# Optimization experiments

Measured on AMD Instinct MI355X. Metric: run time of the kernel, lower is better.

The kernel has to match this reference:

```python
import jax, jax.numpy as jnp
import numpy as np

B, S, D = 8, 2048, 512
KD = 64          # key_dim == value_dim
WIDTH = 128      # attention_width
NEG = 1.0e9


def setup_inputs() -> dict:
    key = jax.random.key(0)
    ks = jax.random.split(key, 16)
    glorot_dd = float(np.sqrt(6.0 / (D + KD)))
    glorot_sd = float(np.sqrt(6.0 / (S + KD)))
    u = lambda k, shape, lim: jax.random.uniform(k, shape, jnp.float32, -lim, lim)
    return {
        "x": jax.random.normal(ks[0], (B, S, D), jnp.float32),
        "Wqr": u(ks[1], (D, KD), glorot_dd), "bqr": jnp.zeros((KD,), jnp.float32),
        "Wqi": u(ks[2], (D, KD), glorot_dd), "bqi": jnp.zeros((KD,), jnp.float32),
        "Wkr": u(ks[3], (D, KD), glorot_dd), "bkr": jnp.zeros((KD,), jnp.float32),
        "Wki": u(ks[4], (D, KD), glorot_dd), "bki": jnp.zeros((KD,), jnp.float32),
        "Wv": u(ks[5], (D, KD), glorot_dd),  "bv": jnp.zeros((KD,), jnp.float32),
        "pos_qr": u(ks[6], (S, KD), glorot_sd), "pos_qi": u(ks[7], (S, KD), glorot_sd),
        "pos_kr": u(ks[8], (S, KD), glorot_sd), "pos_ki": u(ks[9], (S, KD), glorot_sd),
        "temperature": jnp.ones((1,), jnp.float32),
    }


def _masks():
    ind = jnp.arange(S)
    band = (jnp.abs(ind[:, None] - ind[None, :]) <= WIDTH).astype(jnp.float32)  # [S,S]
    causal = jnp.tril(jnp.ones((S, S), jnp.float32))                            # [S,S]
    return band, causal


def reference(x, Wqr, bqr, Wqi, bqi, Wkr, bkr, Wki, bki, Wv, bv,
              pos_qr, pos_qi, pos_kr, pos_ki, temperature):
    scale = 1.0 / jnp.sqrt(jnp.float32(KD))
    # complex Q/K via two real Dense layers; Q scaled BEFORE adding interference
    qr = (x @ Wqr + bqr) * scale + pos_qr[None]   # [B,S,KD]
    qi = (x @ Wqi + bqi) * scale + pos_qi[None]
    kr = (x @ Wkr + bkr) + pos_kr[None]
    ki = (x @ Wki + bki) + pos_ki[None]
    v = x @ Wv + bv                                # [B,S,KD]
    # real part of complex Q @ K^T (transpose, not conjugate-transpose)
    scores = (jnp.einsum('bsd,btd->bst', qr, kr)
              - jnp.einsum('bsd,btd->bst', qi, ki)) * scale  # [B,S,S]
    band, causal = _masks()
    scores = scores * band - NEG * (1.0 - band)
    scores = scores * causal - NEG * (1.0 - causal)
    probs = jax.nn.softmax(scores * temperature[0], axis=-1)
    return jnp.einsum('bst,btd->bsd', probs, v)
```

## Files before the change

kernel.cpp:

```cpp
#include <hip/hip_runtime.h>

#define NB 8
#define NS 2048
#define ND 512
#define NKD 64
#define NM (NB*NS)

typedef _Float16 f16x8 __attribute__((ext_vector_type(8)));
typedef float f32x4 __attribute__((ext_vector_type(4)));


__global__ __launch_bounds__(256) void wprep_kernel(
    const float* __restrict__ w0, const float* __restrict__ w1,
    const float* __restrict__ w2, const float* __restrict__ w3,
    const float* __restrict__ w4,
    f16x8* __restrict__ wfrag)
{
    const int t = blockIdx.x * 256 + threadIdx.x;
    const int p    = t >> 12;
    const int nf   = (t >> 10) & 3;
    const int kt   = (t >> 6) & 15;
    const int lane = t & 63;
    const float* __restrict__ W = (p==0)?w0:(p==1)?w1:(p==2)?w2:(p==3)?w3:w4;
    const int n  = nf*16 + (lane & 15);
    const int k0 = kt*32 + (lane >> 4)*8;
    f16x8 v;
    #pragma unroll
    for (int j = 0; j < 8; ++j)
        v[j] = (_Float16)W[(size_t)(k0 + j)*NKD + n];
    wfrag[t] = v;
}

__global__ __launch_bounds__(256) void proj_mfma(
    const float* __restrict__ x,
    const f16x8* __restrict__ wfrag,
    const float* __restrict__ b0, const float* __restrict__ b1,
    const float* __restrict__ b2, const float* __restrict__ b3,
    const float* __restrict__ b4,
    const float* __restrict__ p0, const float* __restrict__ p1,
    const float* __restrict__ p2, const float* __restrict__ p3,
    _Float16* __restrict__ qkri,
    _Float16* __restrict__ vT)
{
    __shared__ __align__(16) _Float16 vtile[64][40];

    const int w    = threadIdx.x >> 6;
    const int lane = threadIdx.x & 63;
    const int half = w & 1;
    const int mt   = blockIdx.x*2 + (w >> 1);
    const int m0   = mt * 16;

    const int col   = lane & 15;
    const int rbase = (lane >> 4) << 2;

    const float* __restrict__ xrow = x + (size_t)(m0 + col) * ND + (lane >> 4)*8;
    const f16x8* __restrict__ wf   = wfrag + lane;
    const int pa = half * 2;

    f32x4 acc[2][4], accv[2];
    #pragma unroll
    for (int pp = 0; pp < 2; ++pp)
        #pragma unroll
        for (int nf = 0; nf < 4; ++nf) acc[pp][nf] = (f32x4){0.f,0.f,0.f,0.f};
    accv[0] = (f32x4){0.f,0.f,0.f,0.f};
    accv[1] = (f32x4){0.f,0.f,0.f,0.f};

    for (int kt = 0; kt < 16; ++kt) {
        float4 xa = *(const float4*)(xrow + kt*32);
        float4 xb = *(const float4*)(xrow + kt*32 + 4);
        f16x8 a;
        a[0]=(_Float16)xa.x; a[1]=(_Float16)xa.y;
        a[2]=(_Float16)xa.z; a[3]=(_Float16)xa.w;
        a[4]=(_Float16)xb.x; a[5]=(_Float16)xb.y;
        a[6]=(_Float16)xb.z; a[7]=(_Float16)xb.w;
        #pragma unroll
        for (int pp = 0; pp < 2; ++pp)
            #pragma unroll
            for (int nf = 0; nf < 4; ++nf) {
                f16x8 b = wf[((pa + pp)*4 + nf)*1024 + kt*64];
                acc[pp][nf] = __builtin_amdgcn_mfma_f32_16x16x32_f16(a, b, acc[pp][nf], 0, 0, 0);
            }
        #pragma unroll
        for (int j = 0; j < 2; ++j) {
            const int nfv = half*2 + j;
            f16x8 b = wf[(16 + nfv)*1024 + kt*64];
            accv[j] = __builtin_amdgcn_mfma_f32_16x16x32_f16(a, b, accv[j], 0, 0, 0);
        }
    }

    const float* biases[5] = {b0, b1, b2, b3, b4};
    const float* poss[4]   = {p0, p1, p2, p3};

    #pragma unroll
    for (int pp = 0; pp < 2; ++pp) {
        const int p = pa + pp;
        _Float16* ob = qkri + ((size_t)p*NM + m0) * NKD;
        #pragma unroll
        for (int nf = 0; nf < 4; ++nf) {
            const int c = nf*16 + col;
            const float bb = biases[p][c];
            #pragma unroll
            for (int r = 0; r < 4; ++r) {
                const int mm = rbase + r;
                const int s  = (m0 + mm) & (NS - 1);
                float t = acc[pp][nf][r] + bb;
                if (p < 2) t = t * 0.125f + poss[p][s*NKD + c];
                else       t = t + poss[p][s*NKD + c];
                ob[(size_t)mm*NKD + c] = (_Float16)t;
            }
        }
    }

    #pragma unroll
    for (int j = 0; j < 2; ++j) {
        const int c = (half*2 + j)*16 + col;
        const float bb = b4[c];
        #pragma unroll
        for (int r = 0; r < 4; ++r) {
            const int sl = (w >> 1)*16 + rbase + r;
            vtile[c][sl] = (_Float16)(accv[j][r] + bb);
        }
    }
    __syncthreads();
    {
        const int t   = threadIdx.x;
        const int d   = t >> 2;
        const int sc  = (t & 3) * 8;
        const int mblk = blockIdx.x * 32;
        const int bidx = mblk >> 11;
        const int sb   = mblk & (NS - 1);
        f16x8 vv = *(const f16x8*)&vtile[d][sc];
        *(f16x8*)&vT[((size_t)bidx*NKD + d)*NS + sb + sc] = vv;
    }
}

#define SST 164
#define OST 68

__global__ __launch_bounds__(256) void attn_mfma(
    const _Float16* __restrict__ qkri,
    const _Float16* __restrict__ vT,
    const float* __restrict__ temp,
    float* __restrict__ out)
{
    __shared__ __align__(16) float scf[16*SST];
    __shared__ __align__(16) float olds[3][16*OST];

    const int tid  = threadIdx.x;
    const int w    = tid >> 6;
    const int lane = tid & 63;
    const int i0   = blockIdx.x * 16;
    const int b    = blockIdx.y;
    const int jb   = i0 - 128;

    const _Float16* __restrict__ qr_g = qkri + ((size_t)0*NM + (size_t)b*NS)*NKD;
    const _Float16* __restrict__ qi_g = qkri + ((size_t)1*NM + (size_t)b*NS)*NKD;
    const _Float16* __restrict__ kr_g = qkri + ((size_t)2*NM + (size_t)b*NS)*NKD;
    const _Float16* __restrict__ ki_g = qkri + ((size_t)3*NM + (size_t)b*NS)*NKD;
    const _Float16* __restrict__ vT_b = vT + (size_t)b*NKD*NS;

    const f16x8 zf = {};
    const int col  = lane & 15;
    const int seg  = lane >> 4;
    const int qg4  = seg * 4;

    const int qrow = i0 + col;
    const int d0   = seg * 8;
    f16x8 aqr[2], aqi[2];
    #pragma unroll
    for (int kt = 0; kt < 2; ++kt) {
        aqr[kt] = *(const f16x8*)&qr_g[(size_t)qrow*NKD + kt*32 + d0];
        f16x8 qi8 = *(const f16x8*)&qi_g[(size_t)qrow*NKD + kt*32 + d0];
        aqi[kt] = -qi8;
    }

    const float sT  = 0.125f * temp[0];
    const int jrmin = -jb;
    const int tA = (w == 0) ? 0 : (2*w + 1);
    const int tB = 2*w + 2;

    for (int t = tA; t <= tB; ++t) {
        const int row = jb + 16*t + col;
        const bool ok = (row >= 0);
        const _Float16* krp = kr_g + (size_t)row*NKD + d0;
        const _Float16* kip = ki_g + (size_t)row*NKD + d0;
        f16x8 bkr0 = ok ? *(const f16x8*)(krp)      : zf;
        f16x8 bkr1 = ok ? *(const f16x8*)(krp + 32) : zf;
        f16x8 bki0 = ok ? *(const f16x8*)(kip)      : zf;
        f16x8 bki1 = ok ? *(const f16x8*)(kip + 32) : zf;
        f32x4 acc = (f32x4){0.f,0.f,0.f,0.f};
        acc = __builtin_amdgcn_mfma_f32_16x16x32_f16(aqr[0], bkr0, acc, 0,0,0);
        acc = __builtin_amdgcn_mfma_f32_16x16x32_f16(aqr[1], bkr1, acc, 0,0,0);
        acc = __builtin_amdgcn_mfma_f32_16x16x32_f16(aqi[0], bki0, acc, 0,0,0);
        acc = __builtin_amdgcn_mfma_f32_16x16x32_f16(aqi[1], bki1, acc, 0,0,0);
        const int jr = 16*t + col;
        #pragma unroll
        for (int r = 0; r < 4; ++r) {
            const int row16 = qg4 + r;
            const bool okm = (jr >= row16) && (jr <= 128 + row16) && (jr >= jrmin);
            scf[(qg4 + r)*SST + jr] = okm ? acc[r]*sT : -1e30f;
        }
    }
    if (w == 0) {
        #pragma unroll
        for (int r = 0; r < 4; ++r)
            scf[(qg4 + r)*SST + 144 + col] = -1e30f;
    }
    __syncthreads();

    const float* srow = &scf[col*SST + seg*40];
    float4 vv[10];
    float m = -3e38f;
    #pragma unroll
    for (int c = 0; c < 10; ++c) {
        vv[c] = *(const float4*)(srow + 4*c);
        m = fmaxf(m, fmaxf(fmaxf(vv[c].x, vv[c].y), fmaxf(vv[c].z, vv[c].w)));
    }
    m = fmaxf(m, __shfl_xor(m, 16));
    m = fmaxf(m, __shfl_xor(m, 32));
    float l = 0.f;
    #pragma unroll
    for (int c = 0; c < 10; ++c) {
        l += __expf(vv[c].x - m) + __expf(vv[c].y - m)
           + __expf(vv[c].z - m) + __expf(vv[c].w - m);
    }
    l += __shfl_xor(l, 16);
    l += __shfl_xor(l, 32);
    const float inv = 1.0f / l;

    f32x4 oacc[4];
    #pragma unroll
    for (int nf = 0; nf < 4; ++nf) oacc[nf] = (f32x4){0.f,0.f,0.f,0.f};

    #pragma unroll
    for (int pass = 0; pass < 2; ++pass) {
        const int kt = (pass == 0) ? w : 4;
        if (pass == 1 && w != 0) break;
        const int sb = 32*kt + seg*8;
        float4 e0 = *(const float4*)&scf[col*SST + sb];
        float4 e1 = *(const float4*)&scf[col*SST + sb + 4];
        f16x8 a;
        a[0] = (_Float16)(__expf(e0.x - m) * inv);
        a[1] = (_Float16)(__expf(e0.y - m) * inv);
        a[2] = (_Float16)(__expf(e0.z - m) * inv);
        a[3] = (_Float16)(__expf(e0.w - m) * inv);
        a[4] = (_Float16)(__expf(e1.x - m) * inv);
        a[5] = (_Float16)(__expf(e1.y - m) * inv);
        a[6] = (_Float16)(__expf(e1.z - m) * inv);
        a[7] = (_Float16)(__expf(e1.w - m) * inv);
        const int k0 = jb + 32*kt + seg*8;
        const bool okv = (k0 >= 0) && (k0 <= NS - 8);
        #pragma unroll
        for (int nf = 0; nf < 4; ++nf) {
            const int d = nf*16 + col;
            f16x8 bv = okv ? *(const f16x8*)&vT_b[(size_t)d*NS + k0] : zf;
            oacc[nf] = __builtin_amdgcn_mfma_f32_16x16x32_f16(a, bv, oacc[nf], 0,0,0);
        }
    }

    if (w > 0) {
        #pragma unroll
        for (int nf = 0; nf < 4; ++nf)
            #pragma unroll
            for (int r = 0; r < 4; ++r)
                olds[w-1][(qg4 + r)*OST + nf*16 + col] = oacc[nf][r];
    }
    __syncthreads();
    if (w == 0) {
        float* ob = out + ((size_t)b*NS + i0)*NKD;
        #pragma unroll
        for (int nf = 0; nf < 4; ++nf)
            #pragma unroll
            for (int r = 0; r < 4; ++r) {
                const int idx = (qg4 + r)*OST + nf*16 + col;
                const float v = oacc[nf][r] + olds[0][idx] + olds[1][idx] + olds[2][idx];
                ob[(size_t)(qg4 + r)*NKD + nf*16 + col] = v;
            }
    }
}

extern "C" void kernel_launch(void* const* d_in, const int* in_sizes, int n_in,
                              void* d_out, int out_size, void* d_ws, size_t ws_size,
                              hipStream_t stream)
{
    const float* x    = (const float*)d_in[0];
    const float* w0   = (const float*)d_in[1];
    const float* b0   = (const float*)d_in[2];
    const float* w1   = (const float*)d_in[3];
    const float* b1   = (const float*)d_in[4];
    const float* w2   = (const float*)d_in[5];
    const float* b2   = (const float*)d_in[6];
    const float* w3   = (const float*)d_in[7];
    const float* b3   = (const float*)d_in[8];
    const float* w4   = (const float*)d_in[9];
    const float* b4   = (const float*)d_in[10];
    const float* p0   = (const float*)d_in[11];
    const float* p1   = (const float*)d_in[12];
    const float* p2   = (const float*)d_in[13];
    const float* p3   = (const float*)d_in[14];
    const float* temp = (const float*)d_in[15];

    char* ws = (char*)d_ws;
    f16x8*    wfrag = (f16x8*)ws;
    _Float16* qkri  = (_Float16*)(ws + 327680);
    _Float16* vT    = (_Float16*)(ws + 327680 + 8388608);

    wprep_kernel<<<80, 256, 0, stream>>>(w0, w1, w2, w3, w4, wfrag);

    proj_mfma<<<512, 256, 0, stream>>>(x, wfrag,
                                       b0, b1, b2, b3, b4,
                                       p0, p1, p2, p3, qkri, vT);

    dim3 gB(NS/16, NB);
    attn_mfma<<<gB, 256, 0, stream>>>(qkri, vT, temp, (float*)d_out);
}
```

Before: 43.71 us.

## Stage K and V tiles in LDS and interleave batches in attention grid

```diff
diff --git a/kernel.cpp b/kernel.cpp
--- a/kernel.cpp
+++ b/kernel.cpp
@@ -136,6 +136,7 @@
 
 #define SST 164
 #define OST 68
+#define VSTR 184
 
 __global__ __launch_bounds__(256) void attn_mfma(
     const _Float16* __restrict__ qkri,
@@ -143,14 +144,20 @@
     const float* __restrict__ temp,
     float* __restrict__ out)
 {
-    __shared__ __align__(16) float scf[16*SST];
-    __shared__ __align__(16) float olds[3][16*OST];
+    extern __shared__ __align__(16) char smem[];
+    _Float16* krs = (_Float16*)smem;
+    _Float16* kis = krs + 9216;
+    _Float16* vs  = kis + 9216;
+    float*    scf = (float*)(vs + 11776);
+    float*    olds = (float*)smem;
 
     const int tid  = threadIdx.x;
     const int w    = tid >> 6;
     const int lane = tid & 63;
-    const int i0   = blockIdx.x * 16;
-    const int b    = blockIdx.y;
+    const int bid  = blockIdx.x;
+    const int b    = bid & 7;
+    const int ix   = bid >> 3;
+    const int i0   = ix * 16;
     const int jb   = i0 - 128;
 
     const _Float16* __restrict__ qr_g = qkri + ((size_t)0*NM + (size_t)b*NS)*NKD;
@@ -164,6 +171,28 @@
     const int seg  = lane >> 4;
     const int qg4  = seg * 4;
 
+    for (int idx = tid; idx < 2*1152; idx += 256) {
+        const int mtx = (idx >= 1152) ? 1 : 0;
+        const int r   = idx - mtx*1152;
+        const int jj  = r >> 3;
+        const int c8  = r & 7;
+        const int row = jb + jj;
+        f16x8 v = {};
+        if (row >= 0)
+            v = *(const f16x8*)&(mtx ? ki_g : kr_g)[(size_t)row*NKD + c8*8];
+        const int t  = jj >> 4, rl = jj & 15;
+        const int kt = c8 >> 2, lh = c8 & 3;
+        ((f16x8*)(mtx ? kis : krs))[(t*2 + kt)*64 + rl + 16*lh] = v;
+    }
+    for (int idx = tid; idx < 64*20; idx += 256) {
+        const int d = idx / 20, c = idx % 20;
+        const int s = jb + c*8;
+        f16x8 v = {};
+        if (s >= 0 && s <= NS - 8)
+            v = *(const f16x8*)&vT_b[(size_t)d*NS + s];
+        *(f16x8*)&vs[d*VSTR + c*8] = v;
+    }
+
     const int qrow = i0 + col;
     const int d0   = seg * 8;
     f16x8 aqr[2], aqi[2];
@@ -173,6 +202,7 @@
         f16x8 qi8 = *(const f16x8*)&qi_g[(size_t)qrow*NKD + kt*32 + d0];
         aqi[kt] = -qi8;
     }
+    __syncthreads();
 
     const float sT  = 0.125f * temp[0];
     const int jrmin = -jb;
@@ -180,14 +210,10 @@
     const int tB = 2*w + 2;
 
     for (int t = tA; t <= tB; ++t) {
-        const int row = jb + 16*t + col;
-        const bool ok = (row >= 0);
-        const _Float16* krp = kr_g + (size_t)row*NKD + d0;
-        const _Float16* kip = ki_g + (size_t)row*NKD + d0;
-        f16x8 bkr0 = ok ? *(const f16x8*)(krp)      : zf;
-        f16x8 bkr1 = ok ? *(const f16x8*)(krp + 32) : zf;
-        f16x8 bki0 = ok ? *(const f16x8*)(kip)      : zf;
-        f16x8 bki1 = ok ? *(const f16x8*)(kip + 32) : zf;
+        f16x8 bkr0 = ((f16x8*)krs)[(t*2+0)*64 + lane];
+        f16x8 bkr1 = ((f16x8*)krs)[(t*2+1)*64 + lane];
+        f16x8 bki0 = ((f16x8*)kis)[(t*2+0)*64 + lane];
+        f16x8 bki1 = ((f16x8*)kis)[(t*2+1)*64 + lane];
         f32x4 acc = (f32x4){0.f,0.f,0.f,0.f};
         acc = __builtin_amdgcn_mfma_f32_16x16x32_f16(aqr[0], bkr0, acc, 0,0,0);
         acc = __builtin_amdgcn_mfma_f32_16x16x32_f16(aqr[1], bkr1, acc, 0,0,0);
@@ -248,12 +274,10 @@
         a[5] = (_Float16)(__expf(e1.y - m) * inv);
         a[6] = (_Float16)(__expf(e1.z - m) * inv);
         a[7] = (_Float16)(__expf(e1.w - m) * inv);
-        const int k0 = jb + 32*kt + seg*8;
-        const bool okv = (k0 >= 0) && (k0 <= NS - 8);
         #pragma unroll
         for (int nf = 0; nf < 4; ++nf) {
             const int d = nf*16 + col;
-            f16x8 bv = okv ? *(const f16x8*)&vT_b[(size_t)d*NS + k0] : zf;
+            f16x8 bv = *(const f16x8*)&vs[d*VSTR + sb];
             oacc[nf] = __builtin_amdgcn_mfma_f32_16x16x32_f16(a, bv, oacc[nf], 0,0,0);
         }
     }
@@ -263,7 +287,7 @@
         for (int nf = 0; nf < 4; ++nf)
             #pragma unroll
             for (int r = 0; r < 4; ++r)
-                olds[w-1][(qg4 + r)*OST + nf*16 + col] = oacc[nf][r];
+                olds[(w-1)*16*OST + (qg4 + r)*OST + nf*16 + col] = oacc[nf][r];
     }
     __syncthreads();
     if (w == 0) {
@@ -273,11 +297,14 @@
             #pragma unroll
             for (int r = 0; r < 4; ++r) {
                 const int idx = (qg4 + r)*OST + nf*16 + col;
-                const float v = oacc[nf][r] + olds[0][idx] + olds[1][idx] + olds[2][idx];
+                const float v = oacc[nf][r] + olds[idx]
+                              + olds[16*OST + idx] + olds[2*16*OST + idx];
                 ob[(size_t)(qg4 + r)*NKD + nf*16 + col] = v;
             }
     }
 }
+
+#define ATTN_LDS 70912
 
 extern "C" void kernel_launch(void* const* d_in, const int* in_sizes, int n_in,
                               void* d_out, int out_size, void* d_ws, size_t ws_size,
@@ -311,6 +338,7 @@
                                        b0, b1, b2, b3, b4,
                                        p0, p1, p2, p3, qkri, vT);
 
-    dim3 gB(NS/16, NB);
-    attn_mfma<<<gB, 256, 0, stream>>>(qkri, vT, temp, (float*)d_out);
+    hipFuncSetAttribute((const void*)attn_mfma,
+                        hipFuncAttributeMaxDynamicSharedMemorySize, ATTN_LDS);
+    attn_mfma<<<1024, 256, ATTN_LDS, stream>>>(qkri, vT, temp, (float*)d_out);
 }
```

Measured after the change: 48.74 us. 1.12x slower.
